# Kernel optimization log

Measured on AMD Instinct MI355X. Metric: run time of the kernel, lower is better.

The kernel has to match this reference:

```python
import jax, jax.numpy as jnp
import numpy as np

N_NODES = 10000
N_EDGES = 640000
D_FEAT = 128


def setup_inputs() -> dict:
    key = jax.random.key(0)
    k1, k2, k3 = jax.random.split(key, 3)
    feat = jax.random.normal(k1, (N_NODES, D_FEAT), dtype=jnp.float32)
    src = jax.random.randint(k2, (N_EDGES,), 0, N_NODES, dtype=jnp.int64)
    dst = jax.random.randint(k3, (N_EDGES,), 0, N_NODES, dtype=jnp.int64)
    beta = jnp.ones((1,), dtype=jnp.float32)
    return {"feat": feat, "src": src, "dst": dst, "beta": beta}


def reference(feat, src, dst, beta):
    # L2-normalize node features along feature dim (eps matches torch F.normalize)
    norm = feat / jnp.maximum(jnp.linalg.norm(feat, axis=-1, keepdims=True), 1e-12)
    # per-edge cosine similarity: sum over d of norm[src] * norm[dst]  -> [E]
    cos = jnp.einsum('ed,ed->e', norm[src], norm[dst])
    e = beta[0] * cos
    # edge softmax segmented over destination nodes
    seg_max = jax.ops.segment_max(e, dst, num_segments=N_NODES)  # [N]
    ex = jnp.exp(e - seg_max[dst])                               # [E]
    seg_sum = jax.ops.segment_sum(ex, dst, num_segments=N_NODES)  # [N]
    p = ex / seg_sum[dst]                                        # [E]
    # weighted neighbor aggregation: sum_e p_e * feat[src_e] into dst
    msg = feat[src] * p[:, None]                                 # [E, d]
    out = jax.ops.segment_sum(msg, dst, num_segments=N_NODES)    # [N, d]
    return out
```

## Files before the change

kernel.cpp:

```cpp
#include <hip/hip_runtime.h>
#include <math.h>

#define D_FEAT 128
#define EPB_SHIFT 13
#define EPB 8192
#define N_NODES_MAX 10016
#define CAP 128

#define DPP_XOR1 0xB1
#define DPP_XOR2 0x4E
#define DPP_HALF_MIRROR 0x141
#define DPP_MIRROR      0x140

__device__ __forceinline__ unsigned short f2bf(float x) {
    unsigned int b = __float_as_uint(x);
    return (unsigned short)((b + 0x7fffu + ((b >> 16) & 1u)) >> 16);
}
__device__ __forceinline__ float2 bf2_to_f2(unsigned int u) {
    return make_float2(__uint_as_float(u << 16), __uint_as_float(u & 0xffff0000u));
}
template <int CTRL>
__device__ __forceinline__ float dpp_add(float x) {
    int t = __builtin_amdgcn_update_dpp(__float_as_int(x), __float_as_int(x),
                                        CTRL, 0xF, 0xF, false);
    return x + __int_as_float(t);
}

__global__ __launch_bounds__(1024) void hist_norm_kernel(
        const float* __restrict__ feat,
        const int* __restrict__ dst,
        unsigned int* __restrict__ nfb,
        float* __restrict__ invn,
        int* __restrict__ hist,
        unsigned short* __restrict__ lrank,
        int n_nodes, int n_edges, int nbh) {
    __shared__ int lhist[N_NODES_MAX];
    int tid = (int)threadIdx.x;
    if ((int)blockIdx.x < nbh) {
        int b = blockIdx.x;
        for (int i = tid; i < n_nodes; i += 1024) lhist[i] = 0;
        __syncthreads();
        int e0 = b << EPB_SHIFT;
        int e1 = e0 + EPB;
        if (e1 > n_edges) e1 = n_edges;
        for (int e = e0 + tid; e < e1; e += 1024) {
            int d = dst[e];
            lrank[e] = (unsigned short)atomicAdd(&lhist[d], 1);
        }
        __syncthreads();
        for (int i = tid; i < n_nodes; i += 1024)
            hist[b * n_nodes + i] = lhist[i];
    } else {
        int node = ((int)blockIdx.x - nbh) * 16 + (tid >> 6);
        int lane = tid & 63;
        if (node >= n_nodes) return;
        float2 f = ((const float2*)feat)[node * 64 + lane];
        float ss = f.x * f.x + f.y * f.y;
        #pragma unroll
        for (int off = 1; off < 64; off <<= 1)
            ss += __shfl_xor(ss, off, 64);
        unsigned int lo = f2bf(f.x), hi = f2bf(f.y);
        nfb[node * 64 + lane] = (hi << 16) | lo;
        if (lane == 0) invn[node] = 1.0f / fmaxf(sqrtf(ss), 1e-12f);
    }
}

__global__ __launch_bounds__(256) void scan_kernel(int* __restrict__ hist,
                                                   int* __restrict__ cnt,
                                                   int n_nodes, int nbh) {
    int node = (int)(blockIdx.x * blockDim.x + threadIdx.x);
    if (node >= n_nodes) return;
    int base = 0;
    #pragma unroll 8
    for (int b = 0; b < nbh; ++b) {
        int idx = b * n_nodes + node;
        int v = hist[idx];
        hist[idx] = base;
        base += v;
    }
    cnt[node] = base;
}

__global__ __launch_bounds__(256) void scatter_kernel(
        const int* __restrict__ src,
        const int* __restrict__ dst,
        const int* __restrict__ hist,
        const unsigned short* __restrict__ lrank,
        unsigned short* __restrict__ src_sorted,
        int n_nodes, int n_edges) {
    int e = blockIdx.x * blockDim.x + threadIdx.x;
    if (e >= n_edges) return;
    int d = dst[e];
    int b = e >> EPB_SHIFT;
    int r = hist[b * n_nodes + d] + (int)lrank[e];
    if (r < CAP)
        src_sorted[((size_t)d << 7) + r] = (unsigned short)src[e];
}

__global__ void agg_kernel(const unsigned int* __restrict__ nfb,
                           const float* __restrict__ invn,
                           const float* __restrict__ beta,
                           const int* __restrict__ cnt,
                           const unsigned short* __restrict__ src_sorted,
                           float* __restrict__ out, int n_nodes) {
    int node = (int)(blockIdx.x * blockDim.x + threadIdx.x) >> 6;
    int lane = threadIdx.x & 63;
    if (node >= n_nodes) return;
    int deg = cnt[node];
    if (deg > CAP) deg = CAP;
    int beg = node << 7;
    int end = beg + deg;
    int q  = lane >> 4;
    int ql = lane & 15;
    float bd = beta[0] * invn[node];

    uint4 du = ((const uint4*)nfb)[(size_t)node * 16 + ql];
    float2 d0 = bf2_to_f2(du.x), d1 = bf2_to_f2(du.y);
    float2 d2 = bf2_to_f2(du.z), d3 = bf2_to_f2(du.w);

    float l = 0.0f;
    float a0 = 0.f, a1 = 0.f, a2 = 0.f, a3 = 0.f;
    float a4 = 0.f, a5 = 0.f, a6 = 0.f, a7 = 0.f;

    for (int base = beg; base < end; base += 64) {
        int nb = end - base;
        if (nb > 64) nb = 64;
        int gi = base + lane;
        bool valid = gi < end;
        int idx = valid ? (int)src_sorted[gi] : 0;
        float ivm = valid ? invn[idx] * bd : 0.0f;

        #pragma unroll 8
        for (int j = 0; j < nb; j += 4) {
            int jj = j + q;
            int   sj  = __shfl(idx, jj, 64);
            float inj = __shfl(ivm, jj, 64);
            uint4 u = ((const uint4*)nfb)[(size_t)sj * 16 + ql];
            float2 f0 = bf2_to_f2(u.x), f1 = bf2_to_f2(u.y);
            float2 f2 = bf2_to_f2(u.z), f3 = bf2_to_f2(u.w);
            float part = f0.x * d0.x + f0.y * d0.y + f1.x * d1.x + f1.y * d1.y
                       + f2.x * d2.x + f2.y * d2.y + f3.x * d3.x + f3.y * d3.y;
            part = dpp_add<DPP_XOR1>(part);
            part = dpp_add<DPP_XOR2>(part);
            part = dpp_add<DPP_HALF_MIRROR>(part);
            part = dpp_add<DPP_MIRROR>(part);
            float w = __expf(part * inj);
            w = (jj < nb) ? w : 0.0f;
            l += w;
            a0 += w * f0.x;  a1 += w * f0.y;
            a2 += w * f1.x;  a3 += w * f1.y;
            a4 += w * f2.x;  a5 += w * f2.y;
            a6 += w * f3.x;  a7 += w * f3.y;
        }
    }
    #pragma unroll
    for (int off = 1; off < 64; off <<= 1)
        l += __shfl_xor(l, off, 64);
    a0 += __shfl_xor(a0, 16, 64); a0 += __shfl_xor(a0, 32, 64);
    a1 += __shfl_xor(a1, 16, 64); a1 += __shfl_xor(a1, 32, 64);
    a2 += __shfl_xor(a2, 16, 64); a2 += __shfl_xor(a2, 32, 64);
    a3 += __shfl_xor(a3, 16, 64); a3 += __shfl_xor(a3, 32, 64);
    a4 += __shfl_xor(a4, 16, 64); a4 += __shfl_xor(a4, 32, 64);
    a5 += __shfl_xor(a5, 16, 64); a5 += __shfl_xor(a5, 32, 64);
    a6 += __shfl_xor(a6, 16, 64); a6 += __shfl_xor(a6, 32, 64);
    a7 += __shfl_xor(a7, 16, 64); a7 += __shfl_xor(a7, 32, 64);
    float invl = (l > 0.0f) ? (16.0f / l) : 0.0f;
    if (q == 0) {
        float4* o = (float4*)out + (size_t)node * 32 + ql * 2;
        o[0] = make_float4(a0 * invl, a1 * invl, a2 * invl, a3 * invl);
        o[1] = make_float4(a4 * invl, a5 * invl, a6 * invl, a7 * invl);
    }
}

extern "C" void kernel_launch(void* const* d_in, const int* in_sizes, int n_in,
                              void* d_out, int out_size, void* d_ws, size_t ws_size,
                              hipStream_t stream) {
    const float* feat = (const float*)d_in[0];
    const int* src    = (const int*)d_in[1];
    const int* dst    = (const int*)d_in[2];
    const float* beta = (const float*)d_in[3];
    float* out = (float*)d_out;

    const int n_nodes = in_sizes[0] / D_FEAT;
    const int n_edges = in_sizes[1];
    const int nbh = (n_edges + EPB - 1) >> EPB_SHIFT;

    char* ws = (char*)d_ws;
    size_t off = 0;
    auto alloc = [&](size_t bytes) -> void* {
        void* p = ws + off;
        off += (bytes + 255) & ~(size_t)255;
        return p;
    };
    unsigned int*   nfb        = (unsigned int*)alloc((size_t)n_nodes * 64 * 4);
    float*          invn       = (float*)alloc((size_t)n_nodes * 4);
    int*            hist       = (int*)  alloc((size_t)nbh * n_nodes * 4);
    int*            cnt        = (int*)  alloc((size_t)n_nodes * 4);
    unsigned short* lrank      = (unsigned short*)alloc((size_t)n_edges * 2);
    unsigned short* src_sorted = (unsigned short*)alloc((size_t)n_nodes * CAP * 2);

    int nb_norm = (n_nodes + 15) / 16;
    hist_norm_kernel<<<nbh + nb_norm, 1024, 0, stream>>>(
        feat, dst, nfb, invn, hist, lrank, n_nodes, n_edges, nbh);

    scan_kernel<<<(n_nodes + 255) / 256, 256, 0, stream>>>(hist, cnt, n_nodes, nbh);

    scatter_kernel<<<(n_edges + 255) / 256, 256, 0, stream>>>(
        src, dst, hist, lrank, src_sorted, n_nodes, n_edges);

    agg_kernel<<<(n_nodes + 3) / 4, 256, 0, stream>>>(
        nfb, invn, beta, cnt, src_sorted, out, n_nodes);
}
```

Baseline: 112.9 us.

## Fuse histogram, scan and scatter into one cooperative kernel with grid syncs

Replaces the three separate build launches (histogram/normalize, per-node scan, scatter) with a single cooperative kernel of 512 blocks that separates the phases with grid-wide syncs. The intent is to remove kernel launch gaps and inter-kernel drain between the small build stages. The cost is the grid.sync overhead, a fixed block count that must fit co-resident (1024 threads with about 40KB of LDS each), and the scan phase now using only 10 of the 512 blocks. If the cooperative launch fails, the old three-kernel path runs instead.

```diff
diff --git a/kernel.cpp b/kernel.cpp
--- a/kernel.cpp
+++ b/kernel.cpp
@@ -1,11 +1,16 @@
 #include <hip/hip_runtime.h>
+#include <hip/hip_cooperative_groups.h>
 #include <math.h>
+
+namespace cg = cooperative_groups;
 
 #define D_FEAT 128
 #define EPB_SHIFT 13
 #define EPB 8192
 #define N_NODES_MAX 10016
 #define CAP 128
+#define NB_BUILD 512
+
 
 #define DPP_XOR1 0xB1
 #define DPP_XOR2 0x4E
@@ -24,6 +29,76 @@
     int t = __builtin_amdgcn_update_dpp(__float_as_int(x), __float_as_int(x),
                                         CTRL, 0xF, 0xF, false);
     return x + __int_as_float(t);
+}
+
+__global__ __launch_bounds__(1024) void build_kernel(
+        const float* __restrict__ feat,
+        const int* __restrict__ src,
+        const int* __restrict__ dst,
+        unsigned int* __restrict__ nfb,
+        float* __restrict__ invn,
+        int* __restrict__ hist,
+        unsigned short* __restrict__ lrank,
+        unsigned short* __restrict__ src_sorted,
+        int* __restrict__ cnt,
+        int n_nodes, int n_edges, int nbh) {
+    cg::grid_group grid = cg::this_grid();
+    __shared__ int lhist[N_NODES_MAX];
+    const int tid = (int)threadIdx.x;
+    const int bid = (int)blockIdx.x;
+
+    if (bid < nbh) {
+        for (int i = tid; i < n_nodes; i += 1024) lhist[i] = 0;
+        __syncthreads();
+        int e0 = bid << EPB_SHIFT;
+        int e1 = e0 + EPB;
+        if (e1 > n_edges) e1 = n_edges;
+        for (int e = e0 + tid; e < e1; e += 1024) {
+            int d = dst[e];
+            lrank[e] = (unsigned short)atomicAdd(&lhist[d], 1);
+        }
+        __syncthreads();
+        for (int i = tid; i < n_nodes; i += 1024)
+            hist[bid * n_nodes + i] = lhist[i];
+    } else {
+        int lane = tid & 63;
+        for (int node = (bid - nbh) * 16 + (tid >> 6); node < n_nodes;
+             node += (NB_BUILD - nbh) * 16) {
+            float2 f = ((const float2*)feat)[node * 64 + lane];
+            float ss = f.x * f.x + f.y * f.y;
+            #pragma unroll
+            for (int off = 1; off < 64; off <<= 1)
+                ss += __shfl_xor(ss, off, 64);
+            unsigned int lo = f2bf(f.x), hi = f2bf(f.y);
+            nfb[node * 64 + lane] = (hi << 16) | lo;
+            if (lane == 0) invn[node] = 1.0f / fmaxf(sqrtf(ss), 1e-12f);
+        }
+    }
+    grid.sync();
+
+    {
+        int node = bid * 1024 + tid;
+        if (node < n_nodes) {
+            int base = 0;
+            #pragma unroll 8
+            for (int b = 0; b < nbh; ++b) {
+                int idx = b * n_nodes + node;
+                int v = hist[idx];
+                hist[idx] = base;
+                base += v;
+            }
+            cnt[node] = base;
+        }
+    }
+    grid.sync();
+
+    for (int e = bid * 1024 + tid; e < n_edges; e += NB_BUILD * 1024) {
+        int d = dst[e];
+        int b = e >> EPB_SHIFT;
+        int r = hist[b * n_nodes + d] + (int)lrank[e];
+        if (r < CAP)
+            src_sorted[((size_t)d << 7) + r] = (unsigned short)src[e];
+    }
 }
 
 __global__ __launch_bounds__(1024) void hist_norm_kernel(
@@ -199,14 +274,22 @@
     unsigned short* lrank      = (unsigned short*)alloc((size_t)n_edges * 2);
     unsigned short* src_sorted = (unsigned short*)alloc((size_t)n_nodes * CAP * 2);
 
-    int nb_norm = (n_nodes + 15) / 16;
-    hist_norm_kernel<<<nbh + nb_norm, 1024, 0, stream>>>(
-        feat, dst, nfb, invn, hist, lrank, n_nodes, n_edges, nbh);
-
-    scan_kernel<<<(n_nodes + 255) / 256, 256, 0, stream>>>(hist, cnt, n_nodes, nbh);
-
-    scatter_kernel<<<(n_edges + 255) / 256, 256, 0, stream>>>(
-        src, dst, hist, lrank, src_sorted, n_nodes, n_edges);
+    void* args[] = {
+        (void*)&feat, (void*)&src, (void*)&dst, (void*)&nfb, (void*)&invn,
+        (void*)&hist, (void*)&lrank, (void*)&src_sorted, (void*)&cnt,
+        (void*)&n_nodes, (void*)&n_edges, (void*)&nbh };
+    hipError_t err = hipLaunchCooperativeKernel(
+        (const void*)build_kernel, dim3(NB_BUILD), dim3(1024), args, 0, stream);
+
+    if (err != hipSuccess) {
+        int nb_norm = (n_nodes + 15) / 16;
+        hist_norm_kernel<<<nbh + nb_norm, 1024, 0, stream>>>(
+            feat, dst, nfb, invn, hist, lrank, n_nodes, n_edges, nbh);
+        scan_kernel<<<(n_nodes + 255) / 256, 256, 0, stream>>>(
+            hist, cnt, n_nodes, nbh);
+        scatter_kernel<<<(n_edges + 255) / 256, 256, 0, stream>>>(
+            src, dst, hist, lrank, src_sorted, n_nodes, n_edges);
+    }
 
     agg_kernel<<<(n_nodes + 3) / 4, 256, 0, stream>>>(
         nfb, invn, beta, cnt, src_sorted, out, n_nodes);
```

Measured after the change: 240.4 us. 113% more time.
